# Kernel tuning notes

Measured on AMD Instinct MI355X. Metric: run time of the kernel, lower is better.

## Reference

```python
import jax, jax.numpy as jnp
import numpy as np

DIM = 1024
NUM_HEADS = 16
HEAD_DIM = DIM // NUM_HEADS
SCALE = HEAD_DIM ** -0.5


def setup_inputs() -> dict:
    key = jax.random.key(0)
    k1, k2, k3 = jax.random.split(key, 3)
    B, S = 2, 2048
    x = jax.random.normal(k1, (B, S, DIM), dtype=jnp.float32)
    # nn.Linear(dim, 3*dim, bias=False): store as [in, out] for x @ W
    w_qkv = jax.random.normal(k2, (DIM, 3 * DIM), dtype=jnp.float32) * (DIM ** -0.5)
    w_out = jax.random.normal(k3, (DIM, DIM), dtype=jnp.float32) * (DIM ** -0.5)
    return {"x": x, "w_qkv": w_qkv, "w_out": w_out}


def reference(x, w_qkv, w_out):
    B, S, _ = x.shape
    qkv = x @ w_qkv                               # [B,S,3*D]
    q, k, v = jnp.split(qkv, 3, axis=-1)          # each [B,S,D]
    def heads(t):
        return t.reshape(B, S, NUM_HEADS, HEAD_DIM).transpose(0, 2, 1, 3)  # [B,H,S,d]
    q, k, v = heads(q), heads(k), heads(v)
    scores = jnp.einsum('bhqd,bhkd->bhqk', q, k) * SCALE   # [B,H,S,S]
    probs = jax.nn.softmax(scores, axis=-1)
    out = jnp.einsum('bhqk,bhkd->bhqd', probs, v)          # [B,H,S,d]
    out = out.transpose(0, 2, 1, 3).reshape(B, S, DIM)
    return out @ w_out
```

## Files before the change

### kernel.cpp

```cpp
#include <hip/hip_runtime.h>


typedef __bf16 bf16x8 __attribute__((ext_vector_type(8)));
typedef __bf16 bf16x4 __attribute__((ext_vector_type(4)));
typedef float floatx4 __attribute__((ext_vector_type(4)));

#define MFMA16(a, b, c) __builtin_amdgcn_mfma_f32_16x16x32_bf16((a), (b), (c), 0, 0, 0)

__device__ __forceinline__ void gl_lds16(const void* g, void* l) {
  __builtin_amdgcn_global_load_lds((__attribute__((address_space(1))) void*)(g),
                                   (__attribute__((address_space(3))) void*)(l),
                                   16, 0, 0);
}

__global__ __launch_bounds__(256) void prep(const float* __restrict__ x,
                                            const float* __restrict__ w_qkv,
                                            const float* __restrict__ w_out,
                                            __bf16* __restrict__ xb,
                                            __bf16* __restrict__ wqkvt,
                                            __bf16* __restrict__ woutt) {
  __shared__ float tile[64][65];
  const int bid = blockIdx.x, t = threadIdx.x;
  if (bid < 4096) {
    int i = (bid * 256 + t) * 4;
    float4 v = *(const float4*)(x + i);
    bf16x4 o = { (__bf16)v.x, (__bf16)v.y, (__bf16)v.z, (__bf16)v.w };
    *(bf16x4*)(xb + i) = o;
    return;
  }
  const float* w;
  __bf16* wt;
  int K = 1024, N, k0, n0;
  if (bid < 4864) {
    int i = bid - 4096;
    w = w_qkv; wt = wqkvt; N = 3072; k0 = (i & 15) * 64; n0 = (i >> 4) * 64;
  } else {
    int i = bid - 4864;
    w = w_out; wt = woutt; N = 1024; k0 = (i & 15) * 64; n0 = (i >> 4) * 64;
  }
  for (int j = 0; j < 16; ++j) {
    int e = j * 256 + t, r = e >> 6, c = e & 63;
    tile[r][c] = w[(size_t)(k0 + r) * N + n0 + c];
  }
  __syncthreads();
  for (int j = 0; j < 16; ++j) {
    int e = j * 256 + t, r = e >> 6, c = e & 63;
    wt[(size_t)(n0 + r) * K + k0 + c] = (__bf16)tile[c][r];
  }
}

template <typename OutT, bool SPLITV>
__global__ __launch_bounds__(256) void gemm_bt(const __bf16* __restrict__ A,
                                               const __bf16* __restrict__ Bt,
                                               OutT* __restrict__ C,
                                               __bf16* __restrict__ vt, int N) {
  constexpr int K = 1024;
  __shared__ __align__(16) __bf16 aS[128 * 32];
  __shared__ __align__(16) __bf16 bS[128 * 32];
  const int t = threadIdx.x;
  const int lane = t & 63, wave = t >> 6;
  const int l15 = lane & 15, quad = lane >> 4;
  const int wm = wave >> 1, wn = wave & 1;
  const int m0 = blockIdx.y * 128, n0 = blockIdx.x * 128;

  const floatx4 fzero = {0.f, 0.f, 0.f, 0.f};
  floatx4 acc[4][4];
  for (int mt = 0; mt < 4; ++mt)
    for (int nt = 0; nt < 4; ++nt) acc[mt][nt] = fzero;

  const int arow = t >> 2;
  const int ach = ((t & 3) ^ (arow & 3)) * 8;
  const __bf16* gA0 = A + (size_t)(m0 + arow) * K + ach;
  const __bf16* gA1 = gA0 + (size_t)64 * K;
  const __bf16* gB0 = Bt + (size_t)(n0 + arow) * K + ach;
  const __bf16* gB1 = gB0 + (size_t)64 * K;
  const int swz = (quad ^ (l15 & 3)) * 8;

  for (int k0 = 0; k0 < K; k0 += 32) {
    __syncthreads();
    gl_lds16(gA0 + k0, (char*)aS + t * 16);
    gl_lds16(gA1 + k0, (char*)aS + 4096 + t * 16);
    gl_lds16(gB0 + k0, (char*)bS + t * 16);
    gl_lds16(gB1 + k0, (char*)bS + 4096 + t * 16);
    __syncthreads();

    bf16x8 af[4], bfr[4];
    for (int mt = 0; mt < 4; ++mt)
      af[mt] = *(const bf16x8*)(aS + (wm * 64 + mt * 16 + l15) * 32 + swz);
    for (int nt = 0; nt < 4; ++nt)
      bfr[nt] = *(const bf16x8*)(bS + (wn * 64 + nt * 16 + l15) * 32 + swz);
    for (int mt = 0; mt < 4; ++mt)
      for (int nt = 0; nt < 4; ++nt)
        acc[mt][nt] = MFMA16(af[mt], bfr[nt], acc[mt][nt]);
  }

  for (int mt = 0; mt < 4; ++mt) {
    int row = m0 + wm * 64 + mt * 16 + quad * 4;
    for (int nt = 0; nt < 4; ++nt) {
      int col0 = n0 + wn * 64 + nt * 16;
      if (SPLITV && col0 >= 2048) {
        int dfull = col0 + l15 - 2048;
        int bh = ((row >> 11) << 4) + (dfull >> 6);
        int d = dfull & 63, s0 = row & 2047;
        bf16x4 pk = { (__bf16)acc[mt][nt][0], (__bf16)acc[mt][nt][1],
                      (__bf16)acc[mt][nt][2], (__bf16)acc[mt][nt][3] };
        *(bf16x4*)(vt + ((size_t)bh * 64 + d) * 2048 + s0) = pk;
      } else {
        int col = col0 + l15;
        OutT* cp = C + (size_t)row * N + col;
        for (int r = 0; r < 4; ++r) cp[(size_t)r * N] = (OutT)acc[mt][nt][r];
      }
    }
  }
}

__global__ __launch_bounds__(256) void gemm_n64(const __bf16* __restrict__ A,
                                                const __bf16* __restrict__ Bt,
                                                float* __restrict__ C) {
  constexpr int K = 1024, N = 1024;
  __shared__ __align__(16) __bf16 aS[128 * 32];
  __shared__ __align__(16) __bf16 bS[64 * 32];
  const int t = threadIdx.x;
  const int lane = t & 63, wave = t >> 6;
  const int l15 = lane & 15, quad = lane >> 4;
  const int m0 = blockIdx.y * 128, n0 = blockIdx.x * 64;

  const floatx4 fzero = {0.f, 0.f, 0.f, 0.f};
  floatx4 acc[2][4];
  for (int mt = 0; mt < 2; ++mt)
    for (int nt = 0; nt < 4; ++nt) acc[mt][nt] = fzero;

  const int arow = t >> 2;
  const int ach = ((t & 3) ^ (arow & 3)) * 8;
  const __bf16* gA0 = A + (size_t)(m0 + arow) * K + ach;
  const __bf16* gA1 = gA0 + (size_t)64 * K;
  const __bf16* gB0 = Bt + (size_t)(n0 + arow) * K + ach;
  const int swz = (quad ^ (l15 & 3)) * 8;

  for (int k0 = 0; k0 < K; k0 += 32) {
    __syncthreads();
    gl_lds16(gA0 + k0, (char*)aS + t * 16);
    gl_lds16(gA1 + k0, (char*)aS + 4096 + t * 16);
    gl_lds16(gB0 + k0, (char*)bS + t * 16);
    __syncthreads();

    bf16x8 af[2], bfr[4];
    for (int mt = 0; mt < 2; ++mt)
      af[mt] = *(const bf16x8*)(aS + (wave * 32 + mt * 16 + l15) * 32 + swz);
    for (int nt = 0; nt < 4; ++nt)
      bfr[nt] = *(const bf16x8*)(bS + (nt * 16 + l15) * 32 + swz);
    for (int mt = 0; mt < 2; ++mt)
      for (int nt = 0; nt < 4; ++nt)
        acc[mt][nt] = MFMA16(af[mt], bfr[nt], acc[mt][nt]);
  }

  for (int mt = 0; mt < 2; ++mt) {
    int row = m0 + wave * 32 + mt * 16 + quad * 4;
    for (int nt = 0; nt < 4; ++nt) {
      int col = n0 + nt * 16 + l15;
      float* cp = C + (size_t)row * N + col;
      for (int r = 0; r < 4; ++r) cp[(size_t)r * N] = acc[mt][nt][r];
    }
  }
}

__global__ __launch_bounds__(256, 1) void flash_attn(const __bf16* __restrict__ qkv,
                                                     const __bf16* __restrict__ vt,
                                                     __bf16* __restrict__ out) {
  constexpr float SCALE = 0.125f;
  __shared__ __align__(16) __bf16 kS[2 * 64 * 64];
  __shared__ __align__(16) __bf16 vS[2 * 64 * 64];
  __shared__ __align__(16) __bf16 pT[4 * 16 * 64];

  const int t = threadIdx.x;
  const int lane = t & 63, wave = t >> 6;
  const int l15 = lane & 15, quad = lane >> 4;
  const int qb = blockIdx.x, bh = blockIdx.y;
  const int b = bh >> 4, h = bh & 15;

  bf16x8 qf[4][2];
  for (int qt = 0; qt < 4; ++qt) {
    const __bf16* qp = qkv +
        (size_t)(b * 2048 + qb * 256 + wave * 64 + qt * 16 + l15) * 3072 + h * 64 + quad * 8;
    qf[qt][0] = *(const bf16x8*)qp;
    qf[qt][1] = *(const bf16x8*)(qp + 32);
  }

  const floatx4 fzero = {0.f, 0.f, 0.f, 0.f};
  floatx4 oacc[4][4];
  float lsum[4] = {0.f, 0.f, 0.f, 0.f};
  for (int qt = 0; qt < 4; ++qt)
    for (int dt = 0; dt < 4; ++dt) oacc[qt][dt] = fzero;

  const int srow = t >> 3, schk = (t & 7) ^ (srow & 7);
  const __bf16* kg0 =
      qkv + (size_t)(b * 2048 + srow) * 3072 + 1024 + h * 64 + schk * 8;
  const __bf16* kg1 = kg0 + (size_t)32 * 3072;
  const __bf16* vg0 = vt + (size_t)bh * 64 * 2048 + (size_t)srow * 2048 + schk * 8;
  const __bf16* vg1 = vg0 + (size_t)32 * 2048;

  const int l7 = l15 & 7;
  __bf16* pw = pT + wave * 1024 + l15 * 64;

  gl_lds16(kg0, (char*)kS + t * 16);
  gl_lds16(kg1, (char*)kS + 4096 + t * 16);
  gl_lds16(vg0, (char*)vS + t * 16);
  gl_lds16(vg1, (char*)vS + 4096 + t * 16);

  for (int nb = 0; nb < 32; ++nb) {
    __syncthreads();

    if (nb < 31) {
      const size_t n1 = (size_t)(nb + 1) * 64;
      const int oB = ((nb + 1) & 1) * 8192;
      gl_lds16(kg0 + n1 * 3072, (char*)kS + oB + t * 16);
      gl_lds16(kg1 + n1 * 3072, (char*)kS + oB + 4096 + t * 16);
      gl_lds16(vg0 + n1, (char*)vS + oB + t * 16);
      gl_lds16(vg1 + n1, (char*)vS + oB + 4096 + t * 16);
    }

    const __bf16* kC = kS + (nb & 1) * 4096;
    const __bf16* vC = vS + (nb & 1) * 4096;

    bf16x8 kf[4][2];
    for (int nt = 0; nt < 4; ++nt)
      for (int ks = 0; ks < 2; ++ks)
        kf[nt][ks] = *(const bf16x8*)(kC + (nt * 16 + l15) * 64 +
                                      ((ks * 4 + quad) ^ l7) * 8);
    bf16x8 vf[2][4];
    for (int ks = 0; ks < 2; ++ks)
      for (int dt = 0; dt < 4; ++dt)
        vf[ks][dt] = *(const bf16x8*)(vC + (dt * 16 + l15) * 64 +
                                      ((ks * 4 + quad) ^ l7) * 8);

    for (int qt = 0; qt < 4; ++qt) {
      floatx4 sa[4];
      for (int nt = 0; nt < 4; ++nt) {
        floatx4 a = fzero;
        a = MFMA16(kf[nt][0], qf[qt][0], a);
        a = MFMA16(kf[nt][1], qf[qt][1], a);
        sa[nt] = a;
      }
      float ls = 0.f;
      for (int nt = 0; nt < 4; ++nt) {
        float p0 = __expf(sa[nt][0] * SCALE);
        float p1 = __expf(sa[nt][1] * SCALE);
        float p2 = __expf(sa[nt][2] * SCALE);
        float p3 = __expf(sa[nt][3] * SCALE);
        ls += (p0 + p1) + (p2 + p3);
        bf16x4 pk = { (__bf16)p0, (__bf16)p1, (__bf16)p2, (__bf16)p3 };
        *(bf16x4*)(pw + ((nt * 2 + (quad >> 1)) ^ l7) * 8 + (quad & 1) * 4) = pk;
      }
      lsum[qt] += ls;
      for (int ks = 0; ks < 2; ++ks) {
        bf16x8 pa = *(const bf16x8*)(pw + ((ks * 4 + quad) ^ l7) * 8);
        for (int dt = 0; dt < 4; ++dt)
          oacc[qt][dt] = MFMA16(pa, vf[ks][dt], oacc[qt][dt]);
      }
    }
  }

  for (int qt = 0; qt < 4; ++qt) {
    float ls = lsum[qt];
    ls += __shfl_xor(ls, 16);
    ls += __shfl_xor(ls, 32);
    float inv[4];
    for (int r = 0; r < 4; ++r) inv[r] = 1.f / __shfl(ls, quad * 4 + r);
    __bf16* ob = out +
        (size_t)(b * 2048 + qb * 256 + wave * 64 + qt * 16 + quad * 4) * 1024 + h * 64;
    for (int dt = 0; dt < 4; ++dt)
      for (int r = 0; r < 4; ++r)
        ob[(size_t)r * 1024 + dt * 16 + l15] = (__bf16)(oacc[qt][dt][r] * inv[r]);
  }
}

extern "C" void kernel_launch(void* const* d_in, const int* in_sizes, int n_in,
                              void* d_out, int out_size, void* d_ws, size_t ws_size,
                              hipStream_t stream) {
  const float* x = (const float*)d_in[0];
  const float* w_qkv = (const float*)d_in[1];
  const float* w_out = (const float*)d_in[2];
  float* out = (float*)d_out;

  char* ws = (char*)d_ws;
  __bf16* xb = (__bf16*)(ws);
  __bf16* wqkvt = (__bf16*)(ws + ((size_t)8 << 20));
  __bf16* woutt = (__bf16*)(ws + ((size_t)14 << 20));
  __bf16* qkv = (__bf16*)(ws + ((size_t)16 << 20));
  __bf16* vtg = (__bf16*)(ws + ((size_t)40 << 20));
  __bf16* aout = (__bf16*)(ws + ((size_t)48 << 20));

  prep<<<5120, 256, 0, stream>>>(x, w_qkv, w_out, xb, wqkvt, woutt);
  gemm_bt<__bf16, true><<<dim3(24, 32), 256, 0, stream>>>(xb, wqkvt, qkv, vtg, 3072);
  flash_attn<<<dim3(8, 32), 256, 0, stream>>>(qkv, vtg, aout);
  gemm_n64<<<dim3(16, 32), 256, 0, stream>>>(aout, woutt, out);
}
```

Before: 213.9 us.

## Split attention keys across two groups and combine partial outputs in a new kernel

Flash attention now splits the key range into two halves along a new grid dimension. Each block also handles 128 queries instead of 256, so the grid grows from 256 to 1024 blocks, which should fill all CUs with more waves. Each split writes unnormalized fp16 output partials and per-row sums, and a new combine kernel adds them, normalizes, and produces the bf16 attention output. The QKV GEMM now writes only Q and K into a narrower buffer. The cost is an extra launch and extra global traffic for the partials, plus some risk to fp16 range and precision on the unnormalized accumulators.

```diff
diff --git a/kernel.cpp b/kernel.cpp
--- a/kernel.cpp
+++ b/kernel.cpp
@@ -4,6 +4,8 @@
 typedef __bf16 bf16x8 __attribute__((ext_vector_type(8)));
 typedef __bf16 bf16x4 __attribute__((ext_vector_type(4)));
 typedef float floatx4 __attribute__((ext_vector_type(4)));
+typedef _Float16 f16x4 __attribute__((ext_vector_type(4)));
+typedef _Float16 f16x8 __attribute__((ext_vector_type(8)));
 
 #define MFMA16(a, b, c) __builtin_amdgcn_mfma_f32_16x16x32_bf16((a), (b), (c), 0, 0, 0)
 
@@ -49,11 +51,10 @@
   }
 }
 
-template <typename OutT, bool SPLITV>
-__global__ __launch_bounds__(256) void gemm_bt(const __bf16* __restrict__ A,
-                                               const __bf16* __restrict__ Bt,
-                                               OutT* __restrict__ C,
-                                               __bf16* __restrict__ vt, int N) {
+__global__ __launch_bounds__(256) void gemm_qkv(const __bf16* __restrict__ A,
+                                                const __bf16* __restrict__ Bt,
+                                                __bf16* __restrict__ qkb,
+                                                __bf16* __restrict__ vt) {
   constexpr int K = 1024;
   __shared__ __align__(16) __bf16 aS[128 * 32];
   __shared__ __align__(16) __bf16 bS[128 * 32];
@@ -98,7 +99,7 @@
     int row = m0 + wm * 64 + mt * 16 + quad * 4;
     for (int nt = 0; nt < 4; ++nt) {
       int col0 = n0 + wn * 64 + nt * 16;
-      if (SPLITV && col0 >= 2048) {
+      if (col0 >= 2048) {
         int dfull = col0 + l15 - 2048;
         int bh = ((row >> 11) << 4) + (dfull >> 6);
         int d = dfull & 63, s0 = row & 2047;
@@ -107,8 +108,8 @@
         *(bf16x4*)(vt + ((size_t)bh * 64 + d) * 2048 + s0) = pk;
       } else {
         int col = col0 + l15;
-        OutT* cp = C + (size_t)row * N + col;
-        for (int r = 0; r < 4; ++r) cp[(size_t)r * N] = (OutT)acc[mt][nt][r];
+        __bf16* cp = qkb + (size_t)row * 2048 + col;
+        for (int r = 0; r < 4; ++r) cp[(size_t)r * 2048] = (__bf16)acc[mt][nt][r];
       }
     }
   }
@@ -164,9 +165,10 @@
   }
 }
 
-__global__ __launch_bounds__(256, 1) void flash_attn(const __bf16* __restrict__ qkv,
-                                                     const __bf16* __restrict__ vt,
-                                                     __bf16* __restrict__ out) {
+__global__ __launch_bounds__(256) void flash_attn(const __bf16* __restrict__ qkb,
+                                                  const __bf16* __restrict__ vt,
+                                                  _Float16* __restrict__ oPart,
+                                                  float* __restrict__ lPart) {
   constexpr float SCALE = 0.125f;
   __shared__ __align__(16) __bf16 kS[2 * 64 * 64];
   __shared__ __align__(16) __bf16 vS[2 * 64 * 64];
@@ -175,28 +177,29 @@
   const int t = threadIdx.x;
   const int lane = t & 63, wave = t >> 6;
   const int l15 = lane & 15, quad = lane >> 4;
-  const int qb = blockIdx.x, bh = blockIdx.y;
+  const int qb = blockIdx.x, bh = blockIdx.y, grp = blockIdx.z;
   const int b = bh >> 4, h = bh & 15;
 
-  bf16x8 qf[4][2];
-  for (int qt = 0; qt < 4; ++qt) {
-    const __bf16* qp = qkv +
-        (size_t)(b * 2048 + qb * 256 + wave * 64 + qt * 16 + l15) * 3072 + h * 64 + quad * 8;
+  bf16x8 qf[2][2];
+  for (int qt = 0; qt < 2; ++qt) {
+    const __bf16* qp = qkb +
+        (size_t)(b * 2048 + qb * 128 + wave * 32 + qt * 16 + l15) * 2048 + h * 64 + quad * 8;
     qf[qt][0] = *(const bf16x8*)qp;
     qf[qt][1] = *(const bf16x8*)(qp + 32);
   }
 
   const floatx4 fzero = {0.f, 0.f, 0.f, 0.f};
-  floatx4 oacc[4][4];
-  float lsum[4] = {0.f, 0.f, 0.f, 0.f};
-  for (int qt = 0; qt < 4; ++qt)
+  floatx4 oacc[2][4];
+  float lsum[2] = {0.f, 0.f};
+  for (int qt = 0; qt < 2; ++qt)
     for (int dt = 0; dt < 4; ++dt) oacc[qt][dt] = fzero;
 
   const int srow = t >> 3, schk = (t & 7) ^ (srow & 7);
   const __bf16* kg0 =
-      qkv + (size_t)(b * 2048 + srow) * 3072 + 1024 + h * 64 + schk * 8;
-  const __bf16* kg1 = kg0 + (size_t)32 * 3072;
-  const __bf16* vg0 = vt + (size_t)bh * 64 * 2048 + (size_t)srow * 2048 + schk * 8;
+      qkb + (size_t)(b * 2048 + grp * 1024 + srow) * 2048 + 1024 + h * 64 + schk * 8;
+  const __bf16* kg1 = kg0 + (size_t)32 * 2048;
+  const __bf16* vg0 =
+      vt + (size_t)bh * 64 * 2048 + (size_t)srow * 2048 + grp * 1024 + schk * 8;
   const __bf16* vg1 = vg0 + (size_t)32 * 2048;
 
   const int l7 = l15 & 7;
@@ -207,14 +210,14 @@
   gl_lds16(vg0, (char*)vS + t * 16);
   gl_lds16(vg1, (char*)vS + 4096 + t * 16);
 
-  for (int nb = 0; nb < 32; ++nb) {
-    __syncthreads();
-
-    if (nb < 31) {
+  for (int nb = 0; nb < 16; ++nb) {
+    __syncthreads();
+
+    if (nb < 15) {
       const size_t n1 = (size_t)(nb + 1) * 64;
       const int oB = ((nb + 1) & 1) * 8192;
-      gl_lds16(kg0 + n1 * 3072, (char*)kS + oB + t * 16);
-      gl_lds16(kg1 + n1 * 3072, (char*)kS + oB + 4096 + t * 16);
+      gl_lds16(kg0 + n1 * 2048, (char*)kS + oB + t * 16);
+      gl_lds16(kg1 + n1 * 2048, (char*)kS + oB + 4096 + t * 16);
       gl_lds16(vg0 + n1, (char*)vS + oB + t * 16);
       gl_lds16(vg1 + n1, (char*)vS + oB + 4096 + t * 16);
     }
@@ -233,7 +236,7 @@
         vf[ks][dt] = *(const bf16x8*)(vC + (dt * 16 + l15) * 64 +
                                       ((ks * 4 + quad) ^ l7) * 8);
 
-    for (int qt = 0; qt < 4; ++qt) {
+    for (int qt = 0; qt < 2; ++qt) {
       floatx4 sa[4];
       for (int nt = 0; nt < 4; ++nt) {
         floatx4 a = fzero;
@@ -260,18 +263,35 @@
     }
   }
 
-  for (int qt = 0; qt < 4; ++qt) {
+  _Float16* oP = oPart + (size_t)grp * 4096 * 1024;
+  float* lP = lPart + (size_t)grp * 4096 * 16;
+  for (int qt = 0; qt < 2; ++qt) {
     float ls = lsum[qt];
     ls += __shfl_xor(ls, 16);
     ls += __shfl_xor(ls, 32);
-    float inv[4];
-    for (int r = 0; r < 4; ++r) inv[r] = 1.f / __shfl(ls, quad * 4 + r);
-    __bf16* ob = out +
-        (size_t)(b * 2048 + qb * 256 + wave * 64 + qt * 16 + quad * 4) * 1024 + h * 64;
+    int rowb = qb * 128 + wave * 32 + qt * 16;
+    if (quad == 0)
+      lP[(size_t)(b * 2048 + rowb + l15) * 16 + h] = ls;
+    _Float16* ob = oP + (size_t)(b * 2048 + rowb + quad * 4) * 1024 + h * 64;
     for (int dt = 0; dt < 4; ++dt)
       for (int r = 0; r < 4; ++r)
-        ob[(size_t)r * 1024 + dt * 16 + l15] = (__bf16)(oacc[qt][dt][r] * inv[r]);
-  }
+        ob[(size_t)r * 1024 + dt * 16 + l15] = (_Float16)oacc[qt][dt][r];
+  }
+}
+
+__global__ __launch_bounds__(256) void combine(const _Float16* __restrict__ oPart,
+                                               const float* __restrict__ lPart,
+                                               __bf16* __restrict__ aout) {
+  size_t i = ((size_t)blockIdx.x * 256 + threadIdx.x) * 8;
+  int row = i >> 10, h = (i >> 6) & 15;
+  float l0 = lPart[(size_t)row * 16 + h];
+  float l1 = lPart[(size_t)4096 * 16 + (size_t)row * 16 + h];
+  float inv = 1.f / (l0 + l1);
+  f16x8 a = *(const f16x8*)(oPart + i);
+  f16x8 c = *(const f16x8*)(oPart + (size_t)4096 * 1024 + i);
+  bf16x8 o;
+  for (int j = 0; j < 8; ++j) o[j] = (__bf16)(((float)a[j] + (float)c[j]) * inv);
+  *(bf16x8*)(aout + i) = o;
 }
 
 extern "C" void kernel_launch(void* const* d_in, const int* in_sizes, int n_in,
@@ -285,13 +305,16 @@
   char* ws = (char*)d_ws;
   __bf16* xb = (__bf16*)(ws);
   __bf16* wqkvt = (__bf16*)(ws + ((size_t)8 << 20));
-  __bf16* woutt = (__bf16*)(ws + ((size_t)14 << 20));
-  __bf16* qkv = (__bf16*)(ws + ((size_t)16 << 20));
-  __bf16* vtg = (__bf16*)(ws + ((size_t)40 << 20));
-  __bf16* aout = (__bf16*)(ws + ((size_t)48 << 20));
+  _Float16* oPart = (_Float16*)(ws);
+  __bf16* qkb = (__bf16*)(ws + ((size_t)16 << 20));
+  __bf16* vtg = (__bf16*)(ws + ((size_t)32 << 20));
+  __bf16* aout = (__bf16*)(ws + ((size_t)40 << 20));
+  __bf16* woutt = (__bf16*)(ws + ((size_t)48 << 20));
+  float* lPart = (float*)(ws + ((size_t)50 << 20));
 
   prep<<<5120, 256, 0, stream>>>(x, w_qkv, w_out, xb, wqkvt, woutt);
-  gemm_bt<__bf16, true><<<dim3(24, 32), 256, 0, stream>>>(xb, wqkvt, qkv, vtg, 3072);
-  flash_attn<<<dim3(8, 32), 256, 0, stream>>>(qkv, vtg, aout);
+  gemm_qkv<<<dim3(24, 32), 256, 0, stream>>>(xb, wqkvt, qkb, vtg);
+  flash_attn<<<dim3(16, 32, 2), 256, 0, stream>>>(qkb, vtg, oPart, lPart);
+  combine<<<2048, 256, 0, stream>>>(oPart, lPart, aout);
   gemm_n64<<<dim3(16, 32), 256, 0, stream>>>(aout, woutt, out);
 }
```

Result: faster. 206.5 us (-3.5%).
